# Kernel tuning notes

Hardware: AMD Instinct MI355X
Metric: run time of the kernel (lower is better)

The kernel has to match this reference:

```python
import jax, jax.numpy as jnp
import numpy as np
import math

B, SQ, SKV, H = 8, 1024, 1024, 1024
NH, HD = 16, 64  # num_attention_heads, attention_head_size


def setup_inputs() -> dict:
    key = jax.random.key(0)
    ks = jax.random.split(key, 6)
    s = 1.0 / math.sqrt(H)
    return {
        "hidden_states": jax.random.normal(ks[0], (B, SQ, H), jnp.float32),
        "keyvalue_states": jax.random.normal(ks[1], (B, SKV, H), jnp.float32),
        "attention_mask": jnp.zeros((B, 1, 1, SKV), jnp.float32),
        "Wq": jax.random.normal(ks[2], (H, H), jnp.float32) * s,
        "bq": jnp.zeros((H,), jnp.float32),
        "Wk": jax.random.normal(ks[3], (H, H), jnp.float32) * s,
        "bk": jnp.zeros((H,), jnp.float32),
        "Wv": jax.random.normal(ks[4], (H, H), jnp.float32) * s,
        "bv": jnp.zeros((H,), jnp.float32),
    }


def _split_heads(x):
    # [B, S, H] -> [B, NH, S, HD]
    b, s, _ = x.shape
    return x.reshape(b, s, NH, HD).transpose(0, 2, 1, 3)


def reference(hidden_states, keyvalue_states, attention_mask, Wq, bq, Wk, bk, Wv, bv):
    q = _split_heads(hidden_states @ Wq.T + bq)     # [B, NH, SQ, HD]
    k = _split_heads(keyvalue_states @ Wk.T + bk)   # [B, NH, SKV, HD]
    v = _split_heads(keyvalue_states @ Wv.T + bv)   # [B, NH, SKV, HD]
    scores = jnp.einsum("bhqd,bhkd->bhqk", q, k) / math.sqrt(HD)
    scores = scores + attention_mask                 # additive mask broadcast
    probs = jax.nn.softmax(scores, axis=-1)          # dropout = identity (eval)
    ctx = jnp.einsum("bhqk,bhkd->bhqd", probs, v)
    ctx = ctx.transpose(0, 2, 1, 3).reshape(hidden_states.shape[0], -1, NH * HD)
    return ctx
```

## Files before the change

kernel.cpp:

```cpp
#include <hip/hip_runtime.h>
#include <hip/hip_bf16.h>


typedef __attribute__((ext_vector_type(8))) short short8;
typedef __attribute__((ext_vector_type(4))) short short4v;
typedef __attribute__((ext_vector_type(4))) float f32x4;
typedef __attribute__((ext_vector_type(16))) float f32x16;

#define AS1(p) ((const __attribute__((address_space(1))) void*)(p))
#define AS3(p) ((__attribute__((address_space(3))) void*)(p))

__device__ inline short f2bs(float x) {
    __hip_bfloat16 h = __float2bfloat16(x);
    return *reinterpret_cast<short*>(&h);
}

__global__ __launch_bounds__(256) void cvt_bf16(
    const float* __restrict__ s0, const float* __restrict__ s1,
    const float* __restrict__ s2, const float* __restrict__ s3,
    const float* __restrict__ s4,
    short* __restrict__ d0, short* __restrict__ d1,
    short* __restrict__ d2, short* __restrict__ d3, short* __restrict__ d4)
{
    const float* s; short* d; int n4;
    switch (blockIdx.y) {
        case 0: s = s0; d = d0; n4 = 2097152; break;
        case 1: s = s1; d = d1; n4 = 2097152; break;
        case 2: s = s2; d = d2; n4 = 262144;  break;
        case 3: s = s3; d = d3; n4 = 262144;  break;
        default: s = s4; d = d4; n4 = 262144; break;
    }
    for (int i = blockIdx.x * 256 + threadIdx.x; i < n4; i += gridDim.x * 256) {
        float4 v = ((const float4*)s)[i];
        short4v o;
        o.x = f2bs(v.x); o.y = f2bs(v.y); o.z = f2bs(v.z); o.w = f2bs(v.w);
        ((short4v*)d)[i] = o;
    }
}

__global__ __launch_bounds__(256) void qkv_gemm(
    const short* __restrict__ hsb, const short* __restrict__ kvb,
    const short* __restrict__ wqb, const short* __restrict__ wkb,
    const short* __restrict__ wvb,
    const float* __restrict__ bq, const float* __restrict__ bk,
    const float* __restrict__ bv,
    short* __restrict__ qo, short* __restrict__ ko, short* __restrict__ vo)
{
    const short* A; const short* W; const float* bias; short* dst;
    int z = blockIdx.z;
    if (z == 0)      { A = hsb; W = wqb; bias = bq; dst = qo; }
    else if (z == 1) { A = kvb; W = wkb; bias = bk; dst = ko; }
    else             { A = kvb; W = wvb; bias = bv; dst = vo; }

    __shared__ __align__(16) short As[128 * 64];
    __shared__ __align__(16) short Bs[128 * 64];

    const int t = threadIdx.x;
    const int lane = t & 63;
    const int wave = t >> 6;
    const int lane31 = lane & 31;
    const int hi = lane >> 5;
    const int wm = (wave & 1) * 64;
    const int wn = (wave >> 1) * 64;
    const int m0 = blockIdx.x * 128;
    const int n0 = blockIdx.y * 128;

    f32x16 acc[2][2] = {};

    for (int k0 = 0; k0 < 1024; k0 += 64) {
        #pragma unroll
        for (int i = 0; i < 4; ++i) {
            int c = i * 256 + t;
            int row = c >> 3;
            int gc = (c & 7) ^ (row & 7);
            __builtin_amdgcn_global_load_lds(
                AS1(&A[(size_t)(m0 + row) * 1024 + k0 + gc * 8]), AS3(&As[c * 8]), 16, 0, 0);
            __builtin_amdgcn_global_load_lds(
                AS1(&W[(size_t)(n0 + row) * 1024 + k0 + gc * 8]), AS3(&Bs[c * 8]), 16, 0, 0);
        }
        __syncthreads();

        #pragma unroll
        for (int kc = 0; kc < 4; ++kc) {
            short8 af[2], bf[2];
            #pragma unroll
            for (int mt = 0; mt < 2; ++mt) {
                int rr = wm + mt * 32 + lane31;
                af[mt] = *(short8*)&As[rr * 64 + ((kc * 2 + hi) ^ (rr & 7)) * 8];
            }
            #pragma unroll
            for (int nt = 0; nt < 2; ++nt) {
                int rn = wn + nt * 32 + lane31;
                bf[nt] = *(short8*)&Bs[rn * 64 + ((kc * 2 + hi) ^ (rn & 7)) * 8];
            }
            #pragma unroll
            for (int mt = 0; mt < 2; ++mt)
                #pragma unroll
                for (int nt = 0; nt < 2; ++nt)
                    acc[mt][nt] = __builtin_amdgcn_mfma_f32_32x32x16_bf16(
                        af[mt], bf[nt], acc[mt][nt], 0, 0, 0);
        }
        __syncthreads();
    }

    if (z != 2) {
        #pragma unroll
        for (int nt = 0; nt < 2; ++nt) {
            int col = n0 + wn + nt * 32 + lane31;
            float bb = bias[col];
            int h = col >> 6, d = col & 63;
            #pragma unroll
            for (int mt = 0; mt < 2; ++mt) {
                #pragma unroll
                for (int rg = 0; rg < 4; ++rg) {
                    int m = m0 + wm + mt * 32 + rg * 8 + hi * 4;
                    int b = m >> 10, s = m & 1023;
                    size_t base = (size_t)((b * 16 + h) * 1024 + s) * 64 + d;
                    #pragma unroll
                    for (int r = 0; r < 4; ++r)
                        dst[base + (size_t)r * 64] = f2bs(acc[mt][nt][rg * 4 + r] + bb);
                }
            }
        }
    } else {
        #pragma unroll
        for (int nt = 0; nt < 2; ++nt) {
            int col = n0 + wn + nt * 32 + lane31;
            float bb = bias[col];
            int h = col >> 6, d = col & 63;
            #pragma unroll
            for (int mt = 0; mt < 2; ++mt) {
                #pragma unroll
                for (int rg = 0; rg < 4; ++rg) {
                    int m = m0 + wm + mt * 32 + rg * 8 + hi * 4;
                    int b = m >> 10, s = m & 1023;
                    short4v pk;
                    pk.x = f2bs(acc[mt][nt][rg * 4 + 0] + bb);
                    pk.y = f2bs(acc[mt][nt][rg * 4 + 1] + bb);
                    pk.z = f2bs(acc[mt][nt][rg * 4 + 2] + bb);
                    pk.w = f2bs(acc[mt][nt][rg * 4 + 3] + bb);
                    *(short4v*)&dst[(size_t)((b * 16 + h) * 64 + d) * 1024 + s] = pk;
                }
            }
        }
    }
}

#define LDP 68
#define EXPC 0.18033688011112042f
#define LOG2E 1.4426950408889634f
__global__ __launch_bounds__(256) void attn(
    const short* __restrict__ q, const short* __restrict__ k,
    const short* __restrict__ vt, const float* __restrict__ mask,
    float* __restrict__ out)
{
    __shared__ __align__(16) short Ks[2][64 * 64];
    __shared__ __align__(16) short Vs[2][64 * 64];
    __shared__ __align__(16) short Ps[128 * LDP];
    __shared__ __align__(16) short Ms[1024];

    const int t = threadIdx.x;
    const int lane = t & 63;
    const int wq = t >> 6;
    const int lane31 = lane & 31;
    const int hi = lane >> 5;

    const int id = blockIdx.x;
    const int bh = (id >> 6) * 8 + (id & 7);
    const int qt = (id >> 3) & 7;
    const int b = bh >> 4, h = bh & 15;

    const short* qbase = q + (size_t)(bh * 1024 + qt * 128) * 64;
    const short* kbase = k + (size_t)bh * 1024 * 64;
    const short* vbase = vt + (size_t)bh * 64 * 1024;

    {
        float4 mv = ((const float4*)(mask + b * 1024))[t];
        short4v msv;
        msv.x = f2bs(mv.x * LOG2E);
        msv.y = f2bs(mv.y * LOG2E);
        msv.z = f2bs(mv.z * LOG2E);
        msv.w = f2bs(mv.w * LOG2E);
        *(short4v*)&Ms[t * 4] = msv;
    }

    short8 qf[4];
    #pragma unroll
    for (int kc = 0; kc < 4; ++kc)
        qf[kc] = *(const short8*)&qbase[(size_t)(wq * 32 + lane31) * 64 + kc * 16 + hi * 8];

    #pragma unroll
    for (int i = 0; i < 2; ++i) {
        int c = i * 256 + t;
        int row = c >> 3;
        int gc = (c & 7) ^ (row & 7);
        __builtin_amdgcn_global_load_lds(AS1(kbase + (size_t)row * 64 + gc * 8),
                                         AS3(&Ks[0][c * 8]), 16, 0, 0);
        __builtin_amdgcn_global_load_lds(AS1(vbase + (size_t)row * 1024 + gc * 8),
                                         AS3(&Vs[0][c * 8]), 16, 0, 0);
    }

    f32x16 o_acc[2] = {};
    float l_sum = 0.f;

    for (int kt = 0; kt < 16; ++kt) {
        __syncthreads();
        if (kt < 15) {
            int kv1 = (kt + 1) * 64;
            int nb = (kt + 1) & 1;
            #pragma unroll
            for (int i = 0; i < 2; ++i) {
                int c = i * 256 + t;
                int row = c >> 3;
                int gc = (c & 7) ^ (row & 7);
                __builtin_amdgcn_global_load_lds(
                    AS1(kbase + (size_t)(kv1 + row) * 64 + gc * 8),
                    AS3(&Ks[nb][c * 8]), 16, 0, 0);
                __builtin_amdgcn_global_load_lds(
                    AS1(vbase + (size_t)row * 1024 + kv1 + gc * 8),
                    AS3(&Vs[nb][c * 8]), 16, 0, 0);
            }
        }
        const short* ks_ = Ks[kt & 1];
        const short* vs_ = Vs[kt & 1];
        const int kv0 = kt * 64;

        f32x16 sacc[2] = {};
        #pragma unroll
        for (int kc = 0; kc < 4; ++kc) {
            #pragma unroll
            for (int mt = 0; mt < 2; ++mt) {
                int rr = mt * 32 + lane31;
                short8 ak = *(short8*)&ks_[rr * 64 + ((kc * 2 + hi) ^ (rr & 7)) * 8];
                sacc[mt] = __builtin_amdgcn_mfma_f32_32x32x16_bf16(ak, qf[kc], sacc[mt], 0, 0, 0);
            }
        }

        #pragma unroll
        for (int mt = 0; mt < 2; ++mt) {
            #pragma unroll
            for (int rg = 0; rg < 4; ++rg) {
                int kvl = mt * 32 + rg * 8 + hi * 4;
                int2 mw = *(int2*)&Ms[kv0 + kvl];
                float m0 = __uint_as_float(((unsigned)mw.x) << 16);
                float m1 = __uint_as_float(((unsigned)mw.x) & 0xffff0000u);
                float m2 = __uint_as_float(((unsigned)mw.y) << 16);
                float m3 = __uint_as_float(((unsigned)mw.y) & 0xffff0000u);
                float p0 = exp2f(sacc[mt][rg*4+0] * EXPC + m0);
                float p1 = exp2f(sacc[mt][rg*4+1] * EXPC + m1);
                float p2 = exp2f(sacc[mt][rg*4+2] * EXPC + m2);
                float p3 = exp2f(sacc[mt][rg*4+3] * EXPC + m3);
                l_sum += (p0 + p1) + (p2 + p3);
                unsigned u0 = __float_as_uint(p0) + 0x8000u;
                unsigned u1 = __float_as_uint(p1) + 0x8000u;
                unsigned u2 = __float_as_uint(p2) + 0x8000u;
                unsigned u3 = __float_as_uint(p3) + 0x8000u;
                int2 pk;
                pk.x = (int)__builtin_amdgcn_perm(u1, u0, 0x07060302u);
                pk.y = (int)__builtin_amdgcn_perm(u3, u2, 0x07060302u);
                *(int2*)&Ps[(wq * 32 + lane31) * LDP + kvl] = pk;
            }
        }

        #pragma unroll
        for (int kc = 0; kc < 4; ++kc) {
            short8 ap = *(short8*)&Ps[(wq * 32 + lane31) * LDP + kc * 16 + hi * 8];
            #pragma unroll
            for (int nt = 0; nt < 2; ++nt) {
                int rv = nt * 32 + lane31;
                short8 bv_ = *(short8*)&vs_[rv * 64 + ((kc * 2 + hi) ^ (rv & 7)) * 8];
                o_acc[nt] = __builtin_amdgcn_mfma_f32_32x32x16_bf16(ap, bv_, o_acc[nt], 0, 0, 0);
            }
        }
    }

    l_sum += __shfl_xor(l_sum, 32, 64);
    float invl = 1.f / l_sum;

    #pragma unroll
    for (int rg = 0; rg < 4; ++rg) {
        #pragma unroll
        for (int r = 0; r < 4; ++r) {
            int qrow_l = rg * 8 + hi * 4 + r;
            float lv = __shfl(invl, qrow_l, 64);
            int qrow = qt * 128 + wq * 32 + qrow_l;
            size_t base = (size_t)(b * 1024 + qrow) * 1024 + h * 64;
            #pragma unroll
            for (int nt = 0; nt < 2; ++nt)
                out[base + nt * 32 + lane31] = o_acc[nt][rg * 4 + r] * lv;
        }
    }
}

extern "C" void kernel_launch(void* const* d_in, const int* in_sizes, int n_in,
                              void* d_out, int out_size, void* d_ws, size_t ws_size,
                              hipStream_t stream) {
    const float* hs   = (const float*)d_in[0];
    const float* kvs  = (const float*)d_in[1];
    const float* mask = (const float*)d_in[2];
    const float* Wq   = (const float*)d_in[3];
    const float* bq   = (const float*)d_in[4];
    const float* Wk   = (const float*)d_in[5];
    const float* bk   = (const float*)d_in[6];
    const float* Wv   = (const float*)d_in[7];
    const float* bv   = (const float*)d_in[8];
    float* outp = (float*)d_out;

    const size_t big = (size_t)8 * 1024 * 1024;
    const size_t wsz = (size_t)1024 * 1024;
    short* q_ws  = (short*)d_ws;
    short* k_ws  = q_ws  + big;
    short* vt_ws = k_ws  + big;
    short* hsb   = vt_ws + big;
    short* kvb   = hsb   + big;
    short* wqb   = kvb   + big;
    short* wkb   = wqb   + wsz;
    short* wvb   = wkb   + wsz;

    cvt_bf16<<<dim3(1024, 5), 256, 0, stream>>>(hs, kvs, Wq, Wk, Wv,
                                                hsb, kvb, wqb, wkb, wvb);
    qkv_gemm<<<dim3(64, 8, 3), 256, 0, stream>>>(hsb, kvb, wqb, wkb, wvb,
                                                 bq, bk, bv, q_ws, k_ws, vt_ws);
    attn<<<dim3(1024), 256, 0, stream>>>(q_ws, k_ws, vt_ws, mask, outp);
}
```

Baseline: 269.7 us.

## Keep softmax probabilities in registers via permlane32 swap instead of LDS round-trip

```diff
diff --git a/kernel.cpp b/kernel.cpp
--- a/kernel.cpp
+++ b/kernel.cpp
@@ -6,6 +6,8 @@
 typedef __attribute__((ext_vector_type(4))) short short4v;
 typedef __attribute__((ext_vector_type(4))) float f32x4;
 typedef __attribute__((ext_vector_type(16))) float f32x16;
+typedef __attribute__((ext_vector_type(2))) unsigned uint2v;
+typedef __attribute__((ext_vector_type(4))) int int4v;
 
 #define AS1(p) ((const __attribute__((address_space(1))) void*)(p))
 #define AS3(p) ((__attribute__((address_space(3))) void*)(p))
@@ -146,18 +148,30 @@
     }
 }
 
-#define LDP 68
 #define EXPC 0.18033688011112042f
 #define LOG2E 1.4426950408889634f
-__global__ __launch_bounds__(256) void attn(
+
+__device__ inline uint2v half_swap(unsigned c, unsigned d, int hi) {
+#if __has_builtin(__builtin_amdgcn_permlane32_swap)
+    return __builtin_amdgcn_permlane32_swap(c, d, false, false);
+#else
+    unsigned send = hi ? c : d;
+    unsigned recv = (unsigned)__shfl_xor((int)send, 32, 64);
+    uint2v r;
+    r.x = hi ? recv : c;
+    r.y = hi ? d : recv;
+    return r;
+#endif
+}
+
+__global__ __launch_bounds__(256, 4) void attn(
     const short* __restrict__ q, const short* __restrict__ k,
     const short* __restrict__ vt, const float* __restrict__ mask,
     float* __restrict__ out)
 {
     __shared__ __align__(16) short Ks[2][64 * 64];
     __shared__ __align__(16) short Vs[2][64 * 64];
-    __shared__ __align__(16) short Ps[128 * LDP];
-    __shared__ __align__(16) short Ms[1024];
+    __shared__ __align__(16) float Ems[1024];
 
     const int t = threadIdx.x;
     const int lane = t & 63;
@@ -176,12 +190,10 @@
 
     {
         float4 mv = ((const float4*)(mask + b * 1024))[t];
-        short4v msv;
-        msv.x = f2bs(mv.x * LOG2E);
-        msv.y = f2bs(mv.y * LOG2E);
-        msv.z = f2bs(mv.z * LOG2E);
-        msv.w = f2bs(mv.w * LOG2E);
-        *(short4v*)&Ms[t * 4] = msv;
+        float4 o4;
+        o4.x = mv.x * LOG2E; o4.y = mv.y * LOG2E;
+        o4.z = mv.z * LOG2E; o4.w = mv.w * LOG2E;
+        *(float4*)&Ems[t * 4] = o4;
     }
 
     short8 qf[4];
@@ -236,35 +248,34 @@
             }
         }
 
+        unsigned pk[2][4][2];
         #pragma unroll
         for (int mt = 0; mt < 2; ++mt) {
             #pragma unroll
             for (int rg = 0; rg < 4; ++rg) {
                 int kvl = mt * 32 + rg * 8 + hi * 4;
-                int2 mw = *(int2*)&Ms[kv0 + kvl];
-                float m0 = __uint_as_float(((unsigned)mw.x) << 16);
-                float m1 = __uint_as_float(((unsigned)mw.x) & 0xffff0000u);
-                float m2 = __uint_as_float(((unsigned)mw.y) << 16);
-                float m3 = __uint_as_float(((unsigned)mw.y) & 0xffff0000u);
-                float p0 = exp2f(sacc[mt][rg*4+0] * EXPC + m0);
-                float p1 = exp2f(sacc[mt][rg*4+1] * EXPC + m1);
-                float p2 = exp2f(sacc[mt][rg*4+2] * EXPC + m2);
-                float p3 = exp2f(sacc[mt][rg*4+3] * EXPC + m3);
+                f32x4 mk = *(const f32x4*)&Ems[kv0 + kvl];
+                float p0 = exp2f(sacc[mt][rg*4+0] * EXPC + mk[0]);
+                float p1 = exp2f(sacc[mt][rg*4+1] * EXPC + mk[1]);
+                float p2 = exp2f(sacc[mt][rg*4+2] * EXPC + mk[2]);
+                float p3 = exp2f(sacc[mt][rg*4+3] * EXPC + mk[3]);
                 l_sum += (p0 + p1) + (p2 + p3);
                 unsigned u0 = __float_as_uint(p0) + 0x8000u;
                 unsigned u1 = __float_as_uint(p1) + 0x8000u;
                 unsigned u2 = __float_as_uint(p2) + 0x8000u;
                 unsigned u3 = __float_as_uint(p3) + 0x8000u;
-                int2 pk;
-                pk.x = (int)__builtin_amdgcn_perm(u1, u0, 0x07060302u);
-                pk.y = (int)__builtin_amdgcn_perm(u3, u2, 0x07060302u);
-                *(int2*)&Ps[(wq * 32 + lane31) * LDP + kvl] = pk;
+                pk[mt][rg][0] = __builtin_amdgcn_perm(u1, u0, 0x07060302u);
+                pk[mt][rg][1] = __builtin_amdgcn_perm(u3, u2, 0x07060302u);
             }
         }
 
         #pragma unroll
         for (int kc = 0; kc < 4; ++kc) {
-            short8 ap = *(short8*)&Ps[(wq * 32 + lane31) * LDP + kc * 16 + hi * 8];
+            const int mt = kc >> 1, glo = (kc & 1) * 2;
+            uint2v s0 = half_swap(pk[mt][glo][0], pk[mt][glo + 1][0], hi);
+            uint2v s1 = half_swap(pk[mt][glo][1], pk[mt][glo + 1][1], hi);
+            int4v fr; fr.x = (int)s0.x; fr.y = (int)s1.x; fr.z = (int)s0.y; fr.w = (int)s1.y;
+            short8 ap = *(short8*)&fr;
             #pragma unroll
             for (int nt = 0; nt < 2; ++nt) {
                 int rv = nt * 32 + lane31;
```

New measurement: 249.5 us. -7.5%, faster.
